# Performance work log

Measured on AMD Instinct MI355X. Metric: run time of the kernel, lower is better.

The kernel has to match this reference:

```python
import jax, jax.numpy as jnp
from jax import lax
import numpy as np

B, C, H, W = 32, 1, 224, 224
F, KS = 64, 7

def setup_inputs() -> dict:
    key = jax.random.key(0)
    k1, k2 = jax.random.split(key)
    x = jax.random.normal(k1, (B, C, H, W), dtype=jnp.float32)
    # torch.rand -> uniform [0,1)
    kernel = jax.random.uniform(k2, (F, KS, KS), dtype=jnp.float32)
    return {"input": x, "kernel": kernel}

def reference(input, kernel):
    # Original: zero-pad by k//2 on all sides, then for each output pixel
    # out[b, f, i, j] = sum(patch[b, 0] * kernel[f]) -> single-input-channel conv.
    ks = kernel.shape[-1]
    pad = ks // 2
    w = kernel[:, None, :, :]  # [F, 1, ks, ks] in OIHW
    out = lax.conv_general_dilated(
        input, w,
        window_strides=(1, 1),
        padding=[(pad, pad), (pad, pad)],
        dimension_numbers=("NCHW", "OIHW", "NCHW"),
    )
    return out  # [B, F, H, W]
```

## Files before the change

kernel.cpp:

```cpp
#include <hip/hip_runtime.h>


#define TILE    32
#define HALO    3
#define LTY     (TILE + 2 * HALO)
#define LTX     40
#define H_      224
#define W_      224
#define B_      32
#define F_      64
#define FB_     32
#define KS_     7

typedef _Float16 half2_t __attribute__((ext_vector_type(2)));

__device__ __forceinline__ float dot2(half2_t a, half2_t b, float c) {
#if __has_builtin(__builtin_amdgcn_fdot2)
    return __builtin_amdgcn_fdot2(a, b, c, false);
#else
    return c + (float)a.x * (float)b.x + (float)a.y * (float)b.y;
#endif
}

__global__ __launch_bounds__(256)
void Conv_58394375356438_kernel(const float* __restrict__ in,
                                const float* __restrict__ wt,
                                float* __restrict__ out)
{
    __shared__ float   tile[LTY * LTX];
    __shared__ half2_t w2lds[FB_ * 32];

    const int blk   = blockIdx.x;
    const int fhalf = blk & 1;
    const int rest  = blk >> 1;
    const int tx    = rest % (W_ / TILE);
    const int ty    = (rest / (W_ / TILE)) % (H_ / TILE);
    const int b     = rest / ((W_ / TILE) * (H_ / TILE));

    const int x0 = tx * TILE;
    const int y0 = ty * TILE;
    const int fb = fhalf * FB_;
    const float* __restrict__ inp = in + b * (H_ * W_);

    for (int i = threadIdx.x; i < LTY * LTX; i += 256) {
        const int ly = i / LTX;
        const int lx = i - ly * LTX;
        const int gy = y0 + ly - HALO;
        const int gx = x0 + lx - HALO;
        float v = 0.0f;
        if (gy >= 0 && gy < H_ && gx >= 0 && gx < W_)
            v = inp[gy * W_ + gx];
        tile[i] = v;
    }

    for (int idx = threadIdx.x; idx < FB_ * 28; idx += 256) {
        const int f   = idx / 28;
        const int t   = idx - f * 28;
        const int row = t >> 2;
        const int j   = t & 3;
        const int kx  = 2 * j;
        const float* wg = wt + (fb + f) * (KS_ * KS_) + row * KS_ + kx;
        const float w0 = wg[0];
        const float w1 = (kx + 1 < KS_) ? wg[1] : 0.0f;
        half2_t h;
        h.x = (_Float16)w0;
        h.y = (_Float16)w1;
        w2lds[f * 32 + t] = h;
    }
    __syncthreads();

    const int r  = threadIdx.x >> 3;
    const int cx = (threadIdx.x & 7) * 4;

    half2_t pairs[KS_][10];
    #pragma unroll
    for (int ky = 0; ky < KS_; ++ky) {
        const int base = (r + ky) * LTX + cx;
        float c[11];
        #pragma unroll
        for (int s = 0; s < 11; ++s) c[s] = tile[base + s];
        #pragma unroll
        for (int s = 0; s < 10; ++s) {
            half2_t h;
            h.x = (_Float16)c[s];
            h.y = (_Float16)c[s + 1];
            pairs[ky][s] = h;
        }
    }

    float* __restrict__ outp =
        out + ((size_t)(b * F_ + fb) * H_ + (y0 + r)) * W_ + (x0 + cx);

    for (int f = 0; f < FB_; ++f) {
        const half2_t* __restrict__ wf = &w2lds[f * 32];
        float a0 = 0.0f, a1 = 0.0f, a2 = 0.0f, a3 = 0.0f;
        #pragma unroll
        for (int ky = 0; ky < KS_; ++ky) {
            #pragma unroll
            for (int j = 0; j < 4; ++j) {
                const half2_t w = wf[ky * 4 + j];
                a0 = dot2(pairs[ky][0 + 2 * j], w, a0);
                a1 = dot2(pairs[ky][1 + 2 * j], w, a1);
                a2 = dot2(pairs[ky][2 + 2 * j], w, a2);
                a3 = dot2(pairs[ky][3 + 2 * j], w, a3);
            }
        }
        float4 v = make_float4(a0, a1, a2, a3);
        *reinterpret_cast<float4*>(outp + (size_t)f * (H_ * W_)) = v;
    }
}

extern "C" void kernel_launch(void* const* d_in, const int* in_sizes, int n_in,
                              void* d_out, int out_size, void* d_ws, size_t ws_size,
                              hipStream_t stream)
{
    const float* in = (const float*)d_in[0];
    const float* wt = (const float*)d_in[1];
    float* out      = (float*)d_out;

    const int grid = B_ * (H_ / TILE) * (W_ / TILE) * (F_ / FB_);
    Conv_58394375356438_kernel<<<grid, 256, 0, stream>>>(in, wt, out);
}
```

Measured before the change: 443.1 us.

## Compute 7x7 conv with MFMA f16 matrix ops instead of dot2 loops

Replaces the per-thread fdot2 accumulation with 16x16x32 f16 MFMA instructions. Filter weights are held as A fragments in registers, and a shared tile of packed half2 input pairs supplies the B fragments. Each block now computes all 64 filters, which halves the grid and removes the duplicate input-tile loads. The trade-off is scalar strided output stores across filter planes, which may coalesce less well than the earlier float4 stores, plus a more complex fragment mapping.

Measured after the change: 435.9 us. About the same (-1.6%).

```diff
diff --git a/kernel.cpp b/kernel.cpp
--- a/kernel.cpp
+++ b/kernel.cpp
@@ -1,112 +1,116 @@
 #include <hip/hip_runtime.h>
+#include <stdint.h>
 
 
-#define TILE    32
-#define HALO    3
-#define LTY     (TILE + 2 * HALO)
-#define LTX     40
-#define H_      224
-#define W_      224
-#define B_      32
-#define F_      64
-#define FB_     32
-#define KS_     7
+#define H_     224
+#define W_     224
+#define B_     32
+#define F_     64
+#define KS_    7
+#define TILE   32
+#define LROWS  40
+#define LPITCH 40
+#define HW_    (H_ * W_)
 
-typedef _Float16 half2_t __attribute__((ext_vector_type(2)));
-
-__device__ __forceinline__ float dot2(half2_t a, half2_t b, float c) {
-#if __has_builtin(__builtin_amdgcn_fdot2)
-    return __builtin_amdgcn_fdot2(a, b, c, false);
-#else
-    return c + (float)a.x * (float)b.x + (float)a.y * (float)b.y;
-#endif
-}
+typedef _Float16 f16x8 __attribute__((ext_vector_type(8)));
+typedef float    f32x4 __attribute__((ext_vector_type(4)));
 
 __global__ __launch_bounds__(256)
 void Conv_58394375356438_kernel(const float* __restrict__ in,
                                 const float* __restrict__ wt,
                                 float* __restrict__ out)
 {
-    __shared__ float   tile[LTY * LTX];
-    __shared__ half2_t w2lds[FB_ * 32];
+    __shared__ uint32_t P[LROWS * LPITCH];
 
-    const int blk   = blockIdx.x;
-    const int fhalf = blk & 1;
-    const int rest  = blk >> 1;
-    const int tx    = rest % (W_ / TILE);
-    const int ty    = (rest / (W_ / TILE)) % (H_ / TILE);
-    const int b     = rest / ((W_ / TILE) * (H_ / TILE));
+    const int blk = blockIdx.x;
+    const int tx  = blk % (W_ / TILE);
+    const int ty  = (blk / (W_ / TILE)) % (H_ / TILE);
+    const int b   = blk / ((W_ / TILE) * (H_ / TILE));
+    const int x0  = tx * TILE;
+    const int y0  = ty * TILE;
 
-    const int x0 = tx * TILE;
-    const int y0 = ty * TILE;
-    const int fb = fhalf * FB_;
-    const float* __restrict__ inp = in + b * (H_ * W_);
+    const float* __restrict__ inp = in + (size_t)b * HW_;
 
-    for (int i = threadIdx.x; i < LTY * LTX; i += 256) {
-        const int ly = i / LTX;
-        const int lx = i - ly * LTX;
-        const int gy = y0 + ly - HALO;
-        const int gx = x0 + lx - HALO;
-        float v = 0.0f;
-        if (gy >= 0 && gy < H_ && gx >= 0 && gx < W_)
-            v = inp[gy * W_ + gx];
-        tile[i] = v;
+    for (int i = threadIdx.x; i < LROWS * LPITCH; i += 256) {
+        const int rr = i / LPITCH;
+        const int jj = i - rr * LPITCH;
+        const int gy = y0 - 3 + rr;
+        const int gx = x0 - 3 + jj;
+        float v0 = 0.0f, v1 = 0.0f;
+        if (gy >= 0 && gy < H_) {
+            const float* row = inp + gy * W_;
+            if (gx >= 0 && gx < W_)         v0 = row[gx];
+            if (gx + 1 >= 0 && gx + 1 < W_) v1 = row[gx + 1];
+        }
+        union { _Float16 h[2]; uint32_t u; } pk;
+        pk.h[0] = (_Float16)v0;
+        pk.h[1] = (_Float16)v1;
+        P[i] = pk.u;
     }
 
-    for (int idx = threadIdx.x; idx < FB_ * 28; idx += 256) {
-        const int f   = idx / 28;
-        const int t   = idx - f * 28;
-        const int row = t >> 2;
-        const int j   = t & 3;
-        const int kx  = 2 * j;
-        const float* wg = wt + (fb + f) * (KS_ * KS_) + row * KS_ + kx;
-        const float w0 = wg[0];
-        const float w1 = (kx + 1 < KS_) ? wg[1] : 0.0f;
-        half2_t h;
-        h.x = (_Float16)w0;
-        h.y = (_Float16)w1;
-        w2lds[f * 32 + t] = h;
-    }
-    __syncthreads();
+    const int lane = threadIdx.x & 63;
+    const int g    = lane >> 4;
+    const int fr   = lane & 15;
 
-    const int r  = threadIdx.x >> 3;
-    const int cx = (threadIdx.x & 7) * 4;
-
-    half2_t pairs[KS_][10];
+    f16x8 afr[4][2];
     #pragma unroll
-    for (int ky = 0; ky < KS_; ++ky) {
-        const int base = (r + ky) * LTX + cx;
-        float c[11];
+    for (int t = 0; t < 4; ++t) {
         #pragma unroll
-        for (int s = 0; s < 11; ++s) c[s] = tile[base + s];
-        #pragma unroll
-        for (int s = 0; s < 10; ++s) {
-            half2_t h;
-            h.x = (_Float16)c[s];
-            h.y = (_Float16)c[s + 1];
-            pairs[ky][s] = h;
+        for (int kf = 0; kf < 2; ++kf) {
+            const int ky = kf * 4 + g;
+            const float* wrow = wt + (t * 16 + fr) * (KS_ * KS_) + ky * KS_;
+            f16x8 a;
+            #pragma unroll
+            for (int kx = 0; kx < 8; ++kx) {
+                const float w = (ky < KS_ && kx < KS_) ? wrow[kx] : 0.0f;
+                a[kx] = (_Float16)w;
+            }
+            afr[t][kf] = a;
         }
     }
 
-    float* __restrict__ outp =
-        out + ((size_t)(b * F_ + fb) * H_ + (y0 + r)) * W_ + (x0 + cx);
+    __syncthreads();
 
-    for (int f = 0; f < FB_; ++f) {
-        const half2_t* __restrict__ wf = &w2lds[f * 32];
-        float a0 = 0.0f, a1 = 0.0f, a2 = 0.0f, a3 = 0.0f;
+    const int wave = threadIdx.x >> 6;
+    const int p    = lane & 15;
+
+    float* __restrict__ outbase =
+        out + ((size_t)(b * F_ + 4 * g) * H_ + y0) * W_ + x0 + p;
+
+    for (int rr = 0; rr < 8; ++rr) {
+        const int r = wave * 8 + rr;
         #pragma unroll
-        for (int ky = 0; ky < KS_; ++ky) {
+        for (int xb = 0; xb < TILE; xb += 16) {
+            const int base0 = (r + g) * LPITCH + xb + p;
+
+            union { f16x8 v; uint32_t u[4]; } b0, b1;
+            b0.u[0] = P[base0 + 0];
+            b0.u[1] = P[base0 + 2];
+            b0.u[2] = P[base0 + 4];
+            b0.u[3] = P[base0 + 6];
+            b1.u[0] = P[base0 + 4 * LPITCH + 0];
+            b1.u[1] = P[base0 + 4 * LPITCH + 2];
+            b1.u[2] = P[base0 + 4 * LPITCH + 4];
+            b1.u[3] = P[base0 + 4 * LPITCH + 6];
+
+            f32x4 acc[4];
             #pragma unroll
-            for (int j = 0; j < 4; ++j) {
-                const half2_t w = wf[ky * 4 + j];
-                a0 = dot2(pairs[ky][0 + 2 * j], w, a0);
-                a1 = dot2(pairs[ky][1 + 2 * j], w, a1);
-                a2 = dot2(pairs[ky][2 + 2 * j], w, a2);
-                a3 = dot2(pairs[ky][3 + 2 * j], w, a3);
+            for (int t = 0; t < 4; ++t) acc[t] = (f32x4){0.f, 0.f, 0.f, 0.f};
+
+            #pragma unroll
+            for (int t = 0; t < 4; ++t) {
+                acc[t] = __builtin_amdgcn_mfma_f32_16x16x32_f16(afr[t][0], b0.v, acc[t], 0, 0, 0);
+                acc[t] = __builtin_amdgcn_mfma_f32_16x16x32_f16(afr[t][1], b1.v, acc[t], 0, 0, 0);
+            }
+
+            #pragma unroll
+            for (int t = 0; t < 4; ++t) {
+                #pragma unroll
+                for (int j = 0; j < 4; ++j) {
+                    outbase[(size_t)(t * 16 + j) * HW_ + r * W_ + xb] = acc[t][j];
+                }
             }
         }
-        float4 v = make_float4(a0, a1, a2, a3);
-        *reinterpret_cast<float4*>(outp + (size_t)f * (H_ * W_)) = v;
     }
 }
 
@@ -118,6 +122,6 @@
     const float* wt = (const float*)d_in[1];
     float* out      = (float*)d_out;
 
-    const int grid = B_ * (H_ / TILE) * (W_ / TILE) * (F_ / FB_);
+    const int grid = B_ * (H_ / TILE) * (W_ / TILE);
     Conv_58394375356438_kernel<<<grid, 256, 0, stream>>>(in, wt, out);
 }
```
